# Performance work log

Measured on AMD Instinct MI355X. Metric: run time of the kernel, lower is better.

Reference implementation:

```python
import jax, jax.numpy as jnp
import numpy as np

B, F, NB, NS, H, W, C, D = 8, 6, 5, 7, 192, 192, 3, 64
LOSS_WEIGHT = 20.0
EPS = 1e-7  # BCE numerical clamp (torch clamps log terms at -100)


def setup_inputs() -> dict:
    key = jax.random.key(0)
    ks = jax.random.split(key, 8)
    return {
        "segmentations": jax.random.uniform(ks[0], (B, F, NB, H, W), jnp.float32),
        "masks": jax.random.uniform(ks[1], (B, F, NS, H, W), jnp.float32),
        "reconstructions": jax.random.normal(ks[2], (B, F, NB, C, H, W), jnp.float32),
        "rec_tgt": jax.random.normal(ks[3], (B, F, C, H, W), jnp.float32),
        "masks_vis": jax.random.uniform(ks[4], (B, F, NS, H, W), jnp.float32),
        "attn_index": jax.random.uniform(ks[5], (B, F, NS, NB), jnp.float32),
        "slots": jax.random.normal(ks[6], (B, F, NS, D), jnp.float32),
        "pred_slots": jax.random.normal(ks[7], (B, F, NS, D), jnp.float32),
    }


def reference(segmentations, masks, reconstructions, rec_tgt, masks_vis,
              attn_index, slots, pred_slots):
    # Loops over buffer(n) x batch(j) x frame(k>=1) x slot(s) collapse to einsums.
    b, f, nb, h, w = segmentations.shape
    ns = masks.shape[2]
    c = rec_tgt.shape[2]

    p = jnp.clip(segmentations[:, 1:], EPS, 1.0 - EPS)      # [b,f-1,nb,h,w]
    t = (masks[:, 1:] > 0.5).astype(p.dtype)                # [b,f-1,ns,h,w]
    vis = (masks_vis[:, 1:] > 0.5).astype(p.dtype)          # [b,f-1,ns,h,w]

    logp = jnp.log(p)
    log1mp = jnp.log1p(-p)
    # BCE(mean over h*w) for every (buffer n, slot s) pair:
    # -mean[t*logp + (1-t)*log(1-p)] = -(einsum(t, logp-log1mp) + sum(log1mp)) / hw
    ce_pos = jnp.einsum('bfnhw,bfshw->bfns', logp - log1mp, t)
    ce_base = jnp.sum(log1mp, axis=(-1, -2))                # [b,f-1,nb]
    bce = -(ce_pos + ce_base[..., None]) / (h * w)          # [b,f-1,nb,ns]

    # masked MSE: sum(vis * (recon - tgt)^2) / C  (vis is 0/1 so vis^2 = vis)
    diff2 = (reconstructions[:, 1:] - rec_tgt[:, 1:, None]) ** 2  # [b,f-1,nb,c,h,w]
    mse = jnp.einsum('bfnchw,bfshw->bfns', diff2, vis) / c

    loss_ns = bce + 0.1 * mse                               # [b,f-1,nb,ns]
    total = jnp.einsum('bfsn,bfns->', attn_index[:, 1:], loss_ns)
    return total / (b * (f - 1) * nb * ns) * LOSS_WEIGHT
```

## Files before the change

### kernel.cpp

```cpp
#include <hip/hip_runtime.h>

#define TPB 256

namespace {
constexpr int B = 8, F = 6, NB = 5, NS = 7, H = 192, W = 192, C = 3;
constexpr int FM1 = F - 1;
constexpr int HW = H * W;
constexpr int HW4 = HW / 4;
constexpr int PAIRS = B * FM1;
constexpr int BLOCKS_PER_PAIR = HW4 / TPB;
constexpr float EPS = 1e-7f;
constexpr float LN2 = 0.69314718055994530942f;
constexpr float K_BCE = LN2 / (float)HW;
constexpr float COEF = 0.1f / (float)C;
}

__device__ __forceinline__ float4 step05(float4 v) {
  return make_float4(v.x > 0.5f ? 1.f : 0.f, v.y > 0.5f ? 1.f : 0.f,
                     v.z > 0.5f ? 1.f : 0.f, v.w > 0.5f ? 1.f : 0.f);
}
__device__ __forceinline__ void fma4(float4& acc, float s, const float4& v) {
  acc.x = fmaf(s, v.x, acc.x); acc.y = fmaf(s, v.y, acc.y);
  acc.z = fmaf(s, v.z, acc.z); acc.w = fmaf(s, v.w, acc.w);
}
__device__ __forceinline__ float clampp(float p) {
  return __builtin_amdgcn_fmed3f(p, EPS, 1.0f - EPS);
}

__global__ __launch_bounds__(TPB) void em_rec_loss_kernel(
    const float* __restrict__ seg,
    const float* __restrict__ masks,
    const float* __restrict__ recon,
    const float* __restrict__ rtgt,
    const float* __restrict__ vis,
    const float* __restrict__ attn,
    float* __restrict__ out)
{
  const int blk = blockIdx.x;
  const int pair = blk / BLOCKS_PER_PAIR;
  const int chunk = blk - pair * BLOCKS_PER_PAIR;
  const int b = pair / FM1;
  const int f = pair - b * FM1 + 1;
  const int bf = b * F + f;

  float aw[NS][NB], av[NS][NB];
  const float* at = attn + (size_t)bf * NS * NB;
  #pragma unroll
  for (int s = 0; s < NS; ++s)
    #pragma unroll
    for (int n = 0; n < NB; ++n) {
      const float a = at[s * NB + n];
      aw[s][n] = a * K_BCE;
      av[s][n] = a * COEF;
    }
  float AK[NB];
  #pragma unroll
  for (int n = 0; n < NB; ++n) {
    float t = 0.f;
    #pragma unroll
    for (int s = 0; s < NS; ++s) t += aw[s][n];
    AK[n] = t;
  }

  const float4* sp = (const float4*)(seg   + (size_t)bf * NB * HW);
  const float4* mp = (const float4*)(masks + (size_t)bf * NS * HW);
  const float4* vp = (const float4*)(vis   + (size_t)bf * NS * HW);
  const float4* rp = (const float4*)(recon + (size_t)bf * NB * C * HW);
  const float4* tp = (const float4*)(rtgt  + (size_t)bf * C * HW);

  const int q = chunk * TPB + threadIdx.x;

  float4 m4[NS], v4[NS];
  #pragma unroll
  for (int s = 0; s < NS; ++s) m4[s] = mp[s * HW4 + q];
  #pragma unroll
  for (int s = 0; s < NS; ++s) v4[s] = vp[s * HW4 + q];
  float4 tg[C];
  #pragma unroll
  for (int c = 0; c < C; ++c) tg[c] = tp[c * HW4 + q];
  float4 p4[NB];
  #pragma unroll
  for (int n = 0; n < NB; ++n) p4[n] = sp[n * HW4 + q];

  float4 wt[NB], wv[NB];
  #pragma unroll
  for (int n = 0; n < NB; ++n) {
    wt[n] = make_float4(0.f, 0.f, 0.f, 0.f);
    wv[n] = make_float4(0.f, 0.f, 0.f, 0.f);
  }
  #pragma unroll
  for (int s = 0; s < NS; ++s) {
    const float4 t4 = step05(m4[s]);
    const float4 vv = step05(v4[s]);
    #pragma unroll
    for (int n = 0; n < NB; ++n) {
      fma4(wt[n], aw[s][n], t4);
      fma4(wv[n], av[s][n], vv);
    }
  }

  float4 acc4 = make_float4(0.f, 0.f, 0.f, 0.f);
  #pragma unroll
  for (int n = 0; n < NB; ++n) {
    float4 p = p4[n];
    p.x = clampp(p.x); p.y = clampp(p.y); p.z = clampp(p.z); p.w = clampp(p.w);
    const float4 g  = make_float4(__log2f(p.x), __log2f(p.y),
                                  __log2f(p.z), __log2f(p.w));
    const float4 g1 = make_float4(__log2f(1.0f - p.x), __log2f(1.0f - p.y),
                                  __log2f(1.0f - p.z), __log2f(1.0f - p.w));
    float4 d2 = make_float4(0.f, 0.f, 0.f, 0.f);
    #pragma unroll
    for (int c = 0; c < C; ++c) {
      const float4 r = rp[(n * C + c) * HW4 + q];
      const float dx = r.x - tg[c].x, dy = r.y - tg[c].y;
      const float dz = r.z - tg[c].z, dw = r.w - tg[c].w;
      d2.x = fmaf(dx, dx, d2.x); d2.y = fmaf(dy, dy, d2.y);
      d2.z = fmaf(dz, dz, d2.z); d2.w = fmaf(dw, dw, d2.w);
    }
    acc4.x = fmaf(g.x, -wt[n].x, fmaf(g1.x, wt[n].x - AK[n], fmaf(d2.x, wv[n].x, acc4.x)));
    acc4.y = fmaf(g.y, -wt[n].y, fmaf(g1.y, wt[n].y - AK[n], fmaf(d2.y, wv[n].y, acc4.y)));
    acc4.z = fmaf(g.z, -wt[n].z, fmaf(g1.z, wt[n].z - AK[n], fmaf(d2.z, wv[n].z, acc4.z)));
    acc4.w = fmaf(g.w, -wt[n].w, fmaf(g1.w, wt[n].w - AK[n], fmaf(d2.w, wv[n].w, acc4.w)));
  }

  float acc = (acc4.x + acc4.y) + (acc4.z + acc4.w);

  #pragma unroll
  for (int off = 32; off > 0; off >>= 1)
    acc += __shfl_down(acc, off, 64);

  __shared__ float wsum[TPB / 64];
  const int lane = threadIdx.x & 63;
  const int wid = threadIdx.x >> 6;
  if (lane == 0) wsum[wid] = acc;
  __syncthreads();
  if (threadIdx.x == 0) {
    float s = 0.f;
    #pragma unroll
    for (int i = 0; i < TPB / 64; ++i) s += wsum[i];
    constexpr float SCALE = 20.0f / (float)(B * FM1 * NB * NS);
    atomicAdd(out, s * SCALE);
  }
}

extern "C" void kernel_launch(void* const* d_in, const int* in_sizes, int n_in,
                              void* d_out, int out_size, void* d_ws, size_t ws_size,
                              hipStream_t stream) {
  const float* seg   = (const float*)d_in[0];
  const float* masks = (const float*)d_in[1];
  const float* recon = (const float*)d_in[2];
  const float* rtgt  = (const float*)d_in[3];
  const float* vis   = (const float*)d_in[4];
  const float* attn  = (const float*)d_in[5];

  float* out = (float*)d_out;
  hipMemsetAsync(out, 0, sizeof(float), stream);

  const int grid = PAIRS * BLOCKS_PER_PAIR;
  em_rec_loss_kernel<<<grid, TPB, 0, stream>>>(seg, masks, recon, rtgt, vis, attn, out);
}
```

Before: 257.4 us.

## Pre-pack mask and visibility thresholds into bitcodes in a separate kernel

Adds a pre-pass kernel that thresholds the seven mask and seven visibility planes per pixel and packs them into a 16-bit code stored in workspace. The main loss kernel then reads one ushort4 instead of fourteen float4 loads, which cuts its register pressure, and it requests higher occupancy through launch bounds. The trade-off is an extra kernel launch plus the write and re-read of the packed buffer, while the mask and visibility data are still read in full once.

```diff
diff --git a/kernel.cpp b/kernel.cpp
--- a/kernel.cpp
+++ b/kernel.cpp
@@ -8,17 +8,13 @@
 constexpr int HW = H * W;
 constexpr int HW4 = HW / 4;
 constexpr int PAIRS = B * FM1;
-constexpr int BLOCKS_PER_PAIR = HW4 / TPB;
+constexpr int BPP = HW4 / TPB;
 constexpr float EPS = 1e-7f;
 constexpr float LN2 = 0.69314718055994530942f;
 constexpr float K_BCE = LN2 / (float)HW;
 constexpr float COEF = 0.1f / (float)C;
 }
 
-__device__ __forceinline__ float4 step05(float4 v) {
-  return make_float4(v.x > 0.5f ? 1.f : 0.f, v.y > 0.5f ? 1.f : 0.f,
-                     v.z > 0.5f ? 1.f : 0.f, v.w > 0.5f ? 1.f : 0.f);
-}
 __device__ __forceinline__ void fma4(float4& acc, float s, const float4& v) {
   acc.x = fmaf(s, v.x, acc.x); acc.y = fmaf(s, v.y, acc.y);
   acc.z = fmaf(s, v.z, acc.z); acc.w = fmaf(s, v.w, acc.w);
@@ -27,18 +23,56 @@
   return __builtin_amdgcn_fmed3f(p, EPS, 1.0f - EPS);
 }
 
-__global__ __launch_bounds__(TPB) void em_rec_loss_kernel(
+__global__ __launch_bounds__(TPB) void pack_bits(
+    const float* __restrict__ masks,
+    const float* __restrict__ vis,
+    ushort* __restrict__ bm)
+{
+  const int blk = blockIdx.x;
+  const int pair = blk / BPP;
+  const int chunk = blk - pair * BPP;
+  const int b = pair / FM1;
+  const int f = pair - b * FM1 + 1;
+  const int bf = b * F + f;
+
+  const float4* mp = (const float4*)(masks + (size_t)bf * NS * HW);
+  const float4* vp = (const float4*)(vis   + (size_t)bf * NS * HW);
+  const int q = chunk * TPB + threadIdx.x;
+
+  float4 m4[NS], v4[NS];
+  #pragma unroll
+  for (int s = 0; s < NS; ++s) m4[s] = mp[s * HW4 + q];
+  #pragma unroll
+  for (int s = 0; s < NS; ++s) v4[s] = vp[s * HW4 + q];
+
+  unsigned cx = 0, cy = 0, cz = 0, cw = 0;
+  #pragma unroll
+  for (int s = 0; s < NS; ++s) {
+    cx |= ((m4[s].x > 0.5f) ? 1u : 0u) << s;
+    cy |= ((m4[s].y > 0.5f) ? 1u : 0u) << s;
+    cz |= ((m4[s].z > 0.5f) ? 1u : 0u) << s;
+    cw |= ((m4[s].w > 0.5f) ? 1u : 0u) << s;
+    cx |= ((v4[s].x > 0.5f) ? 1u : 0u) << (NS + s);
+    cy |= ((v4[s].y > 0.5f) ? 1u : 0u) << (NS + s);
+    cz |= ((v4[s].z > 0.5f) ? 1u : 0u) << (NS + s);
+    cw |= ((v4[s].w > 0.5f) ? 1u : 0u) << (NS + s);
+  }
+  ushort4 o;
+  o.x = (ushort)cx; o.y = (ushort)cy; o.z = (ushort)cz; o.w = (ushort)cw;
+  ((ushort4*)bm)[(size_t)pair * HW4 + q] = o;
+}
+
+__global__ __launch_bounds__(TPB, 5) void em_rec_loss_kernel(
     const float* __restrict__ seg,
-    const float* __restrict__ masks,
     const float* __restrict__ recon,
     const float* __restrict__ rtgt,
-    const float* __restrict__ vis,
+    const ushort* __restrict__ bm,
     const float* __restrict__ attn,
     float* __restrict__ out)
 {
   const int blk = blockIdx.x;
-  const int pair = blk / BLOCKS_PER_PAIR;
-  const int chunk = blk - pair * BLOCKS_PER_PAIR;
+  const int pair = blk / BPP;
+  const int chunk = blk - pair * BPP;
   const int b = pair / FM1;
   const int f = pair - b * FM1 + 1;
   const int bf = b * F + f;
@@ -63,18 +97,11 @@
   }
 
   const float4* sp = (const float4*)(seg   + (size_t)bf * NB * HW);
-  const float4* mp = (const float4*)(masks + (size_t)bf * NS * HW);
-  const float4* vp = (const float4*)(vis   + (size_t)bf * NS * HW);
   const float4* rp = (const float4*)(recon + (size_t)bf * NB * C * HW);
   const float4* tp = (const float4*)(rtgt  + (size_t)bf * C * HW);
-
   const int q = chunk * TPB + threadIdx.x;
 
-  float4 m4[NS], v4[NS];
-  #pragma unroll
-  for (int s = 0; s < NS; ++s) m4[s] = mp[s * HW4 + q];
-  #pragma unroll
-  for (int s = 0; s < NS; ++s) v4[s] = vp[s * HW4 + q];
+  const ushort4 code = ((const ushort4*)bm)[(size_t)pair * HW4 + q];
   float4 tg[C];
   #pragma unroll
   for (int c = 0; c < C; ++c) tg[c] = tp[c * HW4 + q];
@@ -90,8 +117,15 @@
   }
   #pragma unroll
   for (int s = 0; s < NS; ++s) {
-    const float4 t4 = step05(m4[s]);
-    const float4 vv = step05(v4[s]);
+    float4 t4, vv;
+    t4.x = ((code.x >> s) & 1) ? 1.f : 0.f;
+    t4.y = ((code.y >> s) & 1) ? 1.f : 0.f;
+    t4.z = ((code.z >> s) & 1) ? 1.f : 0.f;
+    t4.w = ((code.w >> s) & 1) ? 1.f : 0.f;
+    vv.x = ((code.x >> (NS + s)) & 1) ? 1.f : 0.f;
+    vv.y = ((code.y >> (NS + s)) & 1) ? 1.f : 0.f;
+    vv.z = ((code.z >> (NS + s)) & 1) ? 1.f : 0.f;
+    vv.w = ((code.w >> (NS + s)) & 1) ? 1.f : 0.f;
     #pragma unroll
     for (int n = 0; n < NB; ++n) {
       fma4(wt[n], aw[s][n], t4);
@@ -154,8 +188,11 @@
   const float* attn  = (const float*)d_in[5];
 
   float* out = (float*)d_out;
+  ushort* bm = (ushort*)d_ws;
+
   hipMemsetAsync(out, 0, sizeof(float), stream);
 
-  const int grid = PAIRS * BLOCKS_PER_PAIR;
-  em_rec_loss_kernel<<<grid, TPB, 0, stream>>>(seg, masks, recon, rtgt, vis, attn, out);
+  const int grid = PAIRS * BPP;
+  pack_bits<<<grid, TPB, 0, stream>>>(masks, vis, bm);
+  em_rec_loss_kernel<<<grid, TPB, 0, stream>>>(seg, recon, rtgt, bm, attn, out);
 }
```

Measured after the change: 277.6 us. 7.8% more time.

## Use single-wave blocks and spread atomics over padded slots with final reduce

Applied to the files above, without the earlier changes.

Blocks shrink to one wavefront, so the shared-memory reduction and barrier are gone and each wave atomically adds its partial to one of 64 slots padded to separate cache lines. A small second kernel sums the slots and writes the scaled result. The goal is to cut contention from thousands of atomics hitting a single address and to remove block-level sync. The cost is four times as many blocks plus an extra kernel launch, and the result now depends on the workspace buffer.

```diff
diff --git a/kernel.cpp b/kernel.cpp
--- a/kernel.cpp
+++ b/kernel.cpp
@@ -1,6 +1,6 @@
 #include <hip/hip_runtime.h>
 
-#define TPB 256
+#define TPB 64
 
 namespace {
 constexpr int B = 8, F = 6, NB = 5, NS = 7, H = 192, W = 192, C = 3;
@@ -8,17 +8,15 @@
 constexpr int HW = H * W;
 constexpr int HW4 = HW / 4;
 constexpr int PAIRS = B * FM1;
-constexpr int BLOCKS_PER_PAIR = HW4 / TPB;
+constexpr int BPP = HW4 / TPB;
+constexpr int NSLOT = 64;
+constexpr int SLOT_STRIDE = 16;
 constexpr float EPS = 1e-7f;
 constexpr float LN2 = 0.69314718055994530942f;
 constexpr float K_BCE = LN2 / (float)HW;
 constexpr float COEF = 0.1f / (float)C;
 }
 
-__device__ __forceinline__ float4 step05(float4 v) {
-  return make_float4(v.x > 0.5f ? 1.f : 0.f, v.y > 0.5f ? 1.f : 0.f,
-                     v.z > 0.5f ? 1.f : 0.f, v.w > 0.5f ? 1.f : 0.f);
-}
 __device__ __forceinline__ void fma4(float4& acc, float s, const float4& v) {
   acc.x = fmaf(s, v.x, acc.x); acc.y = fmaf(s, v.y, acc.y);
   acc.z = fmaf(s, v.z, acc.z); acc.w = fmaf(s, v.w, acc.w);
@@ -26,19 +24,23 @@
 __device__ __forceinline__ float clampp(float p) {
   return __builtin_amdgcn_fmed3f(p, EPS, 1.0f - EPS);
 }
+__device__ __forceinline__ float4 step05(float4 v) {
+  return make_float4(v.x > 0.5f ? 1.f : 0.f, v.y > 0.5f ? 1.f : 0.f,
+                     v.z > 0.5f ? 1.f : 0.f, v.w > 0.5f ? 1.f : 0.f);
+}
 
-__global__ __launch_bounds__(TPB) void em_rec_loss_kernel(
+__global__ __launch_bounds__(TPB, 4) void em_rec_loss_kernel(
     const float* __restrict__ seg,
     const float* __restrict__ masks,
     const float* __restrict__ recon,
     const float* __restrict__ rtgt,
     const float* __restrict__ vis,
     const float* __restrict__ attn,
-    float* __restrict__ out)
+    float* __restrict__ partial)
 {
   const int blk = blockIdx.x;
-  const int pair = blk / BLOCKS_PER_PAIR;
-  const int chunk = blk - pair * BLOCKS_PER_PAIR;
+  const int pair = blk / BPP;
+  const int chunk = blk - pair * BPP;
   const int b = pair / FM1;
   const int f = pair - b * FM1 + 1;
   const int bf = b * F + f;
@@ -129,17 +131,21 @@
   for (int off = 32; off > 0; off >>= 1)
     acc += __shfl_down(acc, off, 64);
 
-  __shared__ float wsum[TPB / 64];
-  const int lane = threadIdx.x & 63;
-  const int wid = threadIdx.x >> 6;
-  if (lane == 0) wsum[wid] = acc;
-  __syncthreads();
   if (threadIdx.x == 0) {
-    float s = 0.f;
-    #pragma unroll
-    for (int i = 0; i < TPB / 64; ++i) s += wsum[i];
+    atomicAdd(&partial[(blk & (NSLOT - 1)) * SLOT_STRIDE], acc);
+  }
+}
+
+__global__ __launch_bounds__(64) void final_reduce(
+    const float* __restrict__ partial, float* __restrict__ out)
+{
+  float v = partial[threadIdx.x * SLOT_STRIDE];
+  #pragma unroll
+  for (int off = 32; off > 0; off >>= 1)
+    v += __shfl_down(v, off, 64);
+  if (threadIdx.x == 0) {
     constexpr float SCALE = 20.0f / (float)(B * FM1 * NB * NS);
-    atomicAdd(out, s * SCALE);
+    out[0] = v * SCALE;
   }
 }
 
@@ -154,8 +160,12 @@
   const float* attn  = (const float*)d_in[5];
 
   float* out = (float*)d_out;
-  hipMemsetAsync(out, 0, sizeof(float), stream);
+  float* partial = (float*)d_ws;
 
-  const int grid = PAIRS * BLOCKS_PER_PAIR;
-  em_rec_loss_kernel<<<grid, TPB, 0, stream>>>(seg, masks, recon, rtgt, vis, attn, out);
+  hipMemsetAsync(partial, 0, NSLOT * SLOT_STRIDE * sizeof(float), stream);
+
+  const int grid = PAIRS * BPP;
+  em_rec_loss_kernel<<<grid, TPB, 0, stream>>>(seg, masks, recon, rtgt, vis,
+                                               attn, partial);
+  final_reduce<<<1, 64, 0, stream>>>(partial, out);
 }
```

Result: no change. 260.2 us (+1.1%).
